# Performance work log

Hardware: AMD Instinct MI355X
Metric: run time of the kernel (lower is better)

## Reference

```python
import jax, jax.numpy as jnp
import numpy as np

STRIDE = 1
PADDING = 1
DILATION = 1


def _conv_one(xi, wi):
    # xi: [C_in, H, W], wi: [C_out, C_in, ks, ks]
    out = jax.lax.conv_general_dilated(
        xi[None],  # [1, C_in, H, W]
        wi,
        window_strides=(STRIDE, STRIDE),
        padding=[(PADDING, PADDING), (PADDING, PADDING)],
        rhs_dilation=(DILATION, DILATION),
        dimension_numbers=("NCHW", "OIHW", "NCHW"),
    )
    return out[0]  # [C_out, H', W']


def setup_inputs() -> dict:
    key = jax.random.key(0)
    k1, k2, k3 = jax.random.split(key, 3)
    B, C_in, C_out, H, W, ks = 32, 32, 32, 256, 256, 3
    x = jax.random.normal(k1, (B, C_in, H, W), dtype=jnp.float32)
    weight = jax.random.normal(k2, (B, C_out, C_in, ks, ks), dtype=jnp.float32)
    bias = jax.random.normal(k3, (B, C_out), dtype=jnp.float32)
    return {"x": x, "weight": weight, "bias": bias}


def reference(x, weight, bias):
    # Per-sample conv: sample i of x convolved with weight[i].
    out = jax.vmap(_conv_one)(x, weight)  # [B, C_out, H', W']
    out = out + bias[:, :, None, None]
    return out
```

## Files before the change

### kernel.cpp

```cpp
#include <hip/hip_runtime.h>


#define BB 32
#define CI 32
#define CO 32
#define HH 256
#define WW 256

typedef unsigned int uint;
using short8  = __attribute__((ext_vector_type(8))) short;
using float4v = __attribute__((ext_vector_type(4))) float;

__device__ inline unsigned short f2bf(float f) {
    union { float f; uint u; } c; c.f = f;
    uint r = c.u + 0x7fffu + ((c.u >> 16) & 1u);
    return (unsigned short)(r >> 16);
}

__global__ __launch_bounds__(256)
void wconv_kernel(const float* __restrict__ wgt,
                  unsigned short* __restrict__ wb) {
    const int i = blockIdx.x * 256 + threadIdx.x;
    const int bc  = i / 288;
    const int rem = i - bc * 288;
    const int ci  = rem / 9;
    const int tap = rem - ci * 9;
    wb[(bc * 9 + tap) * CI + ci] = f2bf(wgt[i]);
}

#define TH 8
#define TW 32
#define XR (TH + 2)
#define XC (TW + 2)

__device__ inline int swz_us(int pix, int q) {
    return pix * CI + (((q ^ (pix >> 1)) & 3) << 3);
}

__global__ __launch_bounds__(256)
void conv_fused_kernel(const float* __restrict__ x,
                       const unsigned short* __restrict__ wb,
                       const float* __restrict__ bias,
                       float* __restrict__ out) {
    __shared__ __align__(16) unsigned short xs[XR * XC * CI];

    const int tw = blockIdx.x;
    const int th = blockIdx.y;
    const int b  = blockIdx.z;
    const int t  = threadIdx.x;
    const int h0 = th * TH, w0 = tw * TW;

    const int wv  = t >> 6;
    const int l   = t & 63;
    const int lp  = l & 15;
    const int lq  = l >> 4;

    const unsigned short* wbb = wb + (size_t)(b * CO) * 9 * CI;
    short8 A0[9], A1[9];
    #pragma unroll
    for (int tp = 0; tp < 9; ++tp) {
        A0[tp] = *(const short8*)(wbb + ((lp)      * 9 + tp) * CI + lq * 8);
        A1[tp] = *(const short8*)(wbb + ((16 + lp) * 9 + tp) * CI + lq * 8);
    }

    const float* xb = x + (size_t)b * CI * HH * WW;
    for (int i = t; i < 1600; i += 256) {
        const int f   = i % 10;
        const int rr  = (i / 10) % 10;
        const int ci2 = i / 100;
        const int ci  = ci2 * 2;
        const int h   = h0 - 1 + rr;
        const int c4  = w0 - 4 + 4 * f;
        float4 va = make_float4(0.f, 0.f, 0.f, 0.f);
        float4 vc = make_float4(0.f, 0.f, 0.f, 0.f);
        if (h >= 0 && h < HH && c4 >= 0 && c4 < WW) {
            const float* p0 = xb + (size_t)ci * HH * WW + (size_t)h * WW + c4;
            va = *(const float4*)p0;
            vc = *(const float4*)(p0 + (size_t)HH * WW);
        }
        const float ae[4] = {va.x, va.y, va.z, va.w};
        const float ce[4] = {vc.x, vc.y, vc.z, vc.w};
        #pragma unroll
        for (int e = 0; e < 4; ++e) {
            const int cl = 4 * f + e - 3;
            if (cl >= 0 && cl < XC) {
                const int p = rr * XC + cl;
                const uint val = (uint)f2bf(ae[e]) | ((uint)f2bf(ce[e]) << 16);
                const int idx = p * CI + (((ci >> 3) ^ ((p >> 1) & 3)) << 3)
                              + (ci & 7);
                *(uint*)(&xs[idx]) = val;
            }
        }
    }
    __syncthreads();

    float4v acc0[4], acc1[4];
    #pragma unroll
    for (int g = 0; g < 4; ++g) {
        acc0[g] = {0.f, 0.f, 0.f, 0.f};
        acc1[g] = {0.f, 0.f, 0.f, 0.f};
    }

    #pragma unroll
    for (int g = 0; g < 4; ++g) {
        const int gg = wv * 4 + g;
        const int r  = gg >> 1;
        const int c0 = (gg & 1) * 16;
        #pragma unroll
        for (int kh = 0; kh < 3; ++kh) {
            #pragma unroll
            for (int kw = 0; kw < 3; ++kw) {
                const int p = (r + kh) * XC + (c0 + lp + kw);
                short8 Bf = *(const short8*)(&xs[swz_us(p, lq)]);
                acc0[g] = __builtin_amdgcn_mfma_f32_16x16x32_bf16(
                    A0[kh * 3 + kw], Bf, acc0[g], 0, 0, 0);
                acc1[g] = __builtin_amdgcn_mfma_f32_16x16x32_bf16(
                    A1[kh * 3 + kw], Bf, acc1[g], 0, 0, 0);
            }
        }
    }

    float bv0[4], bv1[4];
    #pragma unroll
    for (int v = 0; v < 4; ++v) {
        bv0[v] = bias[b * CO + lq * 4 + v];
        bv1[v] = bias[b * CO + 16 + lq * 4 + v];
    }

    #pragma unroll
    for (int g = 0; g < 4; ++g) {
        const int gg = wv * 4 + g;
        const int r  = gg >> 1;
        const int c0 = (gg & 1) * 16;
        const int h  = h0 + r;
        const int wpix = w0 + c0 + lp;
        #pragma unroll
        for (int v = 0; v < 4; ++v) {
            const int co_l = lq * 4 + v;
            out[(((size_t)(b * CO + co_l)) * HH + h) * WW + wpix] =
                acc0[g][v] + bv0[v];
            out[(((size_t)(b * CO + 16 + co_l)) * HH + h) * WW + wpix] =
                acc1[g][v] + bv1[v];
        }
    }
}

#define FHT 16
#define FXR (FHT + 2)
#define LROW 264

__global__ __launch_bounds__(256)
void conv3x3_fallback(const float* __restrict__ x,
                      const float* __restrict__ wgt,
                      const float* __restrict__ bias,
                      float* __restrict__ out) {
    __shared__ float xs[FXR * LROW];
    __shared__ float wsh[CI * 9];
    const int co = blockIdx.x;
    const int ht = blockIdx.y;
    const int b  = blockIdx.z;
    const int tid = threadIdx.x;
    const int h0 = ht * FHT;
    for (int i = tid; i < CI * 9; i += 256)
        wsh[i] = wgt[((size_t)(b * CO + co) * CI) * 9 + i];
    for (int i = tid; i < FXR * 8; i += 256) {
        int row = i >> 3; int c = i & 7;
        int col = (c < 4) ? c : (256 + c);
        xs[row * LROW + col] = 0.0f;
    }
    const int wg = tid & 63, rp = tid >> 6;
    const int w0 = wg * 4, r0 = rp * 4;
    float acc[4][4];
    #pragma unroll
    for (int d = 0; d < 4; ++d)
        #pragma unroll
        for (int j = 0; j < 4; ++j) acc[d][j] = 0.0f;
    const float* xb = x + (size_t)(b * CI) * HH * WW;
    for (int ci = 0; ci < CI; ++ci) {
        __syncthreads();
        const float* xsrc = xb + (size_t)ci * HH * WW;
        for (int i = tid; i < FXR * 64; i += 256) {
            int row = i >> 6; int cq = i & 63;
            int gh = h0 - 1 + row;
            float4 v = make_float4(0.f, 0.f, 0.f, 0.f);
            if (gh >= 0 && gh < HH)
                v = *(const float4*)(xsrc + (size_t)gh * WW + cq * 4);
            *(float4*)(&xs[row * LROW + 4 + cq * 4]) = v;
        }
        __syncthreads();
        float wk[9];
        #pragma unroll
        for (int k = 0; k < 9; ++k) wk[k] = wsh[ci * 9 + k];
        #pragma unroll
        for (int xr = 0; xr < 6; ++xr) {
            const float* rowp = &xs[(r0 + xr) * LROW + w0];
            float xv[12];
            #pragma unroll
            for (int q = 0; q < 3; ++q) {
                float4 v = *(const float4*)(rowp + 4 * q);
                xv[4*q+0] = v.x; xv[4*q+1] = v.y; xv[4*q+2] = v.z; xv[4*q+3] = v.w;
            }
            #pragma unroll
            for (int dr = 0; dr < 4; ++dr) {
                const int kh = xr - dr;
                if (kh < 0 || kh > 2) continue;
                #pragma unroll
                for (int kw = 0; kw < 3; ++kw) {
                    const float wvv = wk[kh * 3 + kw];
                    #pragma unroll
                    for (int j = 0; j < 4; ++j)
                        acc[dr][j] += xv[j + kw + 3] * wvv;
                }
            }
        }
    }
    const float bv = bias[b * CO + co];
    float* ob = out + ((size_t)(b * CO + co) * HH + (h0 + r0)) * WW + w0;
    #pragma unroll
    for (int dr = 0; dr < 4; ++dr) {
        float4 o;
        o.x = acc[dr][0] + bv; o.y = acc[dr][1] + bv;
        o.z = acc[dr][2] + bv; o.w = acc[dr][3] + bv;
        *(float4*)(ob + (size_t)dr * WW) = o;
    }
}

extern "C" void kernel_launch(void* const* d_in, const int* in_sizes, int n_in,
                              void* d_out, int out_size, void* d_ws, size_t ws_size,
                              hipStream_t stream) {
    const float* x    = (const float*)d_in[0];
    const float* wgt  = (const float*)d_in[1];
    const float* bias = (const float*)d_in[2];
    float* out        = (float*)d_out;

    const size_t wb_bytes = (size_t)BB * CO * 9 * CI * sizeof(unsigned short);
    if (ws_size >= wb_bytes) {
        unsigned short* wbp = (unsigned short*)d_ws;
        hipLaunchKernelGGL(wconv_kernel, dim3((BB * CO * CI * 9) / 256), dim3(256),
                           0, stream, wgt, wbp);
        hipLaunchKernelGGL(conv_fused_kernel, dim3(WW / TW, HH / TH, BB), dim3(256),
                           0, stream, x, wbp, bias, out);
    } else {
        hipLaunchKernelGGL(conv3x3_fallback, dim3(CO, HH / FHT, BB), dim3(256),
                           0, stream, x, wgt, bias, out);
    }
}
```

Measured before the change: 503.5 us.

## Double tile height, swap MFMA operands for float4 stores, vectorize staging conversion

Doubles the output tile to 16 rows with 512 threads per block, which halves the halo overhead and the number of weight-register reloads per output. The staging loop now loads 8 channels per thread and packs them with the hardware bf16 pack instruction into one 16-byte shared store, using a padded 40-column row layout. The MFMA operands are swapped so each lane holds 4 consecutive pixels of one output channel. That lets the epilogue write float4 vectors instead of scattered scalar stores. The cost is a larger LDS footprint and more registers per thread at 512 threads, which may lower occupancy.

```diff
diff --git a/kernel.cpp b/kernel.cpp
--- a/kernel.cpp
+++ b/kernel.cpp
@@ -15,6 +15,12 @@
     union { float f; uint u; } c; c.f = f;
     uint r = c.u + 0x7fffu + ((c.u >> 16) & 1u);
     return (unsigned short)(r >> 16);
+}
+
+__device__ inline uint pk2bf(float lo, float hi) {
+    uint r;
+    asm("v_cvt_pk_bf16_f32 %0, %1, %2" : "=v"(r) : "v"(lo), "v"(hi));
+    return r;
 }
 
 __global__ __launch_bounds__(256)
@@ -28,16 +34,16 @@
     wb[(bc * 9 + tap) * CI + ci] = f2bf(wgt[i]);
 }
 
-#define TH 8
+#define TH 16
 #define TW 32
 #define XR (TH + 2)
-#define XC (TW + 2)
+#define XC 40
 
 __device__ inline int swz_us(int pix, int q) {
     return pix * CI + (((q ^ (pix >> 1)) & 3) << 3);
 }
 
-__global__ __launch_bounds__(256)
+__global__ __launch_bounds__(512)
 void conv_fused_kernel(const float* __restrict__ x,
                        const unsigned short* __restrict__ wb,
                        const float* __restrict__ bias,
@@ -56,40 +62,41 @@
     const int lq  = l >> 4;
 
     const unsigned short* wbb = wb + (size_t)(b * CO) * 9 * CI;
-    short8 A0[9], A1[9];
+    short8 W0[9], W1[9];
     #pragma unroll
     for (int tp = 0; tp < 9; ++tp) {
-        A0[tp] = *(const short8*)(wbb + ((lp)      * 9 + tp) * CI + lq * 8);
-        A1[tp] = *(const short8*)(wbb + ((16 + lp) * 9 + tp) * CI + lq * 8);
+        W0[tp] = *(const short8*)(wbb + ((lp)      * 9 + tp) * CI + lq * 8);
+        W1[tp] = *(const short8*)(wbb + ((16 + lp) * 9 + tp) * CI + lq * 8);
     }
 
     const float* xb = x + (size_t)b * CI * HH * WW;
-    for (int i = t; i < 1600; i += 256) {
-        const int f   = i % 10;
-        const int rr  = (i / 10) % 10;
-        const int ci2 = i / 100;
-        const int ci  = ci2 * 2;
+    for (int i = t; i < XR * 10 * 4; i += 512) {
+        const int qd  = i / 10;
+        const int f   = i - qd * 10;
+        const int ciq = qd & 3;
+        const int rr  = qd >> 2;
         const int h   = h0 - 1 + rr;
         const int c4  = w0 - 4 + 4 * f;
-        float4 va = make_float4(0.f, 0.f, 0.f, 0.f);
-        float4 vc = make_float4(0.f, 0.f, 0.f, 0.f);
-        if (h >= 0 && h < HH && c4 >= 0 && c4 < WW) {
-            const float* p0 = xb + (size_t)ci * HH * WW + (size_t)h * WW + c4;
-            va = *(const float4*)p0;
-            vc = *(const float4*)(p0 + (size_t)HH * WW);
-        }
-        const float ae[4] = {va.x, va.y, va.z, va.w};
-        const float ce[4] = {vc.x, vc.y, vc.z, vc.w};
+        float4v v[8];
+        if (h >= 0 && h < HH && c4 >= 0 && c4 <= WW - 4) {
+            const float* p0 = xb + (size_t)(ciq * 8) * HH * WW
+                                 + (size_t)h * WW + c4;
+            #pragma unroll
+            for (int j = 0; j < 8; ++j)
+                v[j] = *(const float4v*)(p0 + (size_t)j * HH * WW);
+        } else {
+            #pragma unroll
+            for (int j = 0; j < 8; ++j) v[j] = {0.f, 0.f, 0.f, 0.f};
+        }
         #pragma unroll
         for (int e = 0; e < 4; ++e) {
-            const int cl = 4 * f + e - 3;
-            if (cl >= 0 && cl < XC) {
-                const int p = rr * XC + cl;
-                const uint val = (uint)f2bf(ae[e]) | ((uint)f2bf(ce[e]) << 16);
-                const int idx = p * CI + (((ci >> 3) ^ ((p >> 1) & 3)) << 3)
-                              + (ci & 7);
-                *(uint*)(&xs[idx]) = val;
-            }
+            const int p = rr * XC + 4 * f + e;
+            uint4 pk;
+            pk.x = pk2bf(v[0][e], v[1][e]);
+            pk.y = pk2bf(v[2][e], v[3][e]);
+            pk.z = pk2bf(v[4][e], v[5][e]);
+            pk.w = pk2bf(v[6][e], v[7][e]);
+            *(uint4*)(&xs[swz_us(p, ciq)]) = pk;
         }
     }
     __syncthreads();
@@ -110,22 +117,18 @@
         for (int kh = 0; kh < 3; ++kh) {
             #pragma unroll
             for (int kw = 0; kw < 3; ++kw) {
-                const int p = (r + kh) * XC + (c0 + lp + kw);
-                short8 Bf = *(const short8*)(&xs[swz_us(p, lq)]);
+                const int p = (r + kh) * XC + (c0 + lp + kw + 3);
+                short8 Pf = *(const short8*)(&xs[swz_us(p, lq)]);
                 acc0[g] = __builtin_amdgcn_mfma_f32_16x16x32_bf16(
-                    A0[kh * 3 + kw], Bf, acc0[g], 0, 0, 0);
+                    Pf, W0[kh * 3 + kw], acc0[g], 0, 0, 0);
                 acc1[g] = __builtin_amdgcn_mfma_f32_16x16x32_bf16(
-                    A1[kh * 3 + kw], Bf, acc1[g], 0, 0, 0);
+                    Pf, W1[kh * 3 + kw], acc1[g], 0, 0, 0);
             }
         }
     }
 
-    float bv0[4], bv1[4];
-    #pragma unroll
-    for (int v = 0; v < 4; ++v) {
-        bv0[v] = bias[b * CO + lq * 4 + v];
-        bv1[v] = bias[b * CO + 16 + lq * 4 + v];
-    }
+    const float bv0 = bias[b * CO + lp];
+    const float bv1 = bias[b * CO + 16 + lp];
 
     #pragma unroll
     for (int g = 0; g < 4; ++g) {
@@ -133,15 +136,11 @@
         const int r  = gg >> 1;
         const int c0 = (gg & 1) * 16;
         const int h  = h0 + r;
-        const int wpix = w0 + c0 + lp;
-        #pragma unroll
-        for (int v = 0; v < 4; ++v) {
-            const int co_l = lq * 4 + v;
-            out[(((size_t)(b * CO + co_l)) * HH + h) * WW + wpix] =
-                acc0[g][v] + bv0[v];
-            out[(((size_t)(b * CO + 16 + co_l)) * HH + h) * WW + wpix] =
-                acc1[g][v] + bv1[v];
-        }
+        const int wb4 = w0 + c0 + lq * 4;
+        float4v o0 = acc0[g] + bv0;
+        float4v o1 = acc1[g] + bv1;
+        *(float4v*)(&out[(((size_t)(b * CO + lp)) * HH + h) * WW + wb4]) = o0;
+        *(float4v*)(&out[(((size_t)(b * CO + 16 + lp)) * HH + h) * WW + wb4]) = o1;
     }
 }
 
@@ -238,7 +237,7 @@
         unsigned short* wbp = (unsigned short*)d_ws;
         hipLaunchKernelGGL(wconv_kernel, dim3((BB * CO * CI * 9) / 256), dim3(256),
                            0, stream, wgt, wbp);
-        hipLaunchKernelGGL(conv_fused_kernel, dim3(WW / TW, HH / TH, BB), dim3(256),
+        hipLaunchKernelGGL(conv_fused_kernel, dim3(WW / TW, HH / TH, BB), dim3(512),
                            0, stream, x, wbp, bias, out);
     } else {
         hipLaunchKernelGGL(conv3x3_fallback, dim3(CO, HH / FHT, BB), dim3(256),
```

After: 493.8 us. No clear change (-1.9%).
